# Optimization experiments

Measured on AMD Instinct MI355X. Metric: run time of the kernel, lower is better.

Reference implementation:

```python
import jax, jax.numpy as jnp
import numpy as np

NUM_HEADS = 16
HEAD_DIM = 64
EMB = 1024


def setup_inputs() -> dict:
    key = jax.random.key(0)
    k1, k2, k3 = jax.random.split(key, 3)
    x = jax.random.normal(k1, (4, 1024, EMB), dtype=jnp.float32)
    W_qkv = jax.random.normal(k2, (EMB, 3 * NUM_HEADS * HEAD_DIM), dtype=jnp.float32) * (EMB ** -0.5)
    b_qkv = jnp.zeros((3 * NUM_HEADS * HEAD_DIM,), dtype=jnp.float32)
    W_out = jax.random.normal(k3, (NUM_HEADS * HEAD_DIM, EMB), dtype=jnp.float32) * ((NUM_HEADS * HEAD_DIM) ** -0.5)
    b_out = jnp.zeros((EMB,), dtype=jnp.float32)
    return {"x": x, "W_qkv": W_qkv, "b_qkv": b_qkv, "W_out": W_out, "b_out": b_out}


def reference(x, W_qkv, b_qkv, W_out, b_out):
    B, N, D = x.shape
    qkv = x @ W_qkv + b_qkv                      # B N 3*H*hd
    # torch.split order in the source is K, Q, V
    K, Q, V = jnp.split(qkv, 3, axis=-1)
    def heads(t):  # B N (H hd) -> B H N hd
        return t.reshape(B, N, NUM_HEADS, HEAD_DIM).transpose(0, 2, 1, 3)
    K, Q, V = heads(K), heads(Q), heads(V)
    scores = jnp.einsum('bhqd,bhkd->bhqk', Q, K) / (HEAD_DIM ** 0.5)
    att = jax.nn.softmax(scores, axis=-1)        # dropout p=0.0 -> identity
    out = jnp.einsum('bhqk,bhkd->bhqd', att, V)  # B H N hd
    out = out.transpose(0, 2, 1, 3).reshape(B, N, NUM_HEADS * HEAD_DIM)
    return out @ W_out + b_out
```

## Files before the change

kernel.cpp:

```cpp
#include <hip/hip_runtime.h>
#include <hip/hip_bf16.h>
#include <cstddef>
#include <cmath>


typedef _Float16 f16x4 __attribute__((ext_vector_type(4)));
typedef _Float16 f16x8 __attribute__((ext_vector_type(8)));
typedef float    f32x4 __attribute__((ext_vector_type(4)));

#define LOG2E 1.4426950408889634f

__device__ __forceinline__ void gload_lds16(const void* g, void* l) {
    __builtin_amdgcn_global_load_lds(
        (const __attribute__((address_space(1))) unsigned int*)g,
        (__attribute__((address_space(3))) unsigned int*)l, 16, 0, 0);
}

__global__ __launch_bounds__(256) void cvt_f32_f16(
    const float* __restrict__ in, _Float16* __restrict__ out, int n8)
{
    int i = blockIdx.x * 256 + threadIdx.x;
    if (i < n8) {
        const float4* p = (const float4*)in;
        float4 v0 = p[i * 2], v1 = p[i * 2 + 1];
        f16x8 o;
        o[0] = (_Float16)v0.x; o[1] = (_Float16)v0.y; o[2] = (_Float16)v0.z; o[3] = (_Float16)v0.w;
        o[4] = (_Float16)v1.x; o[5] = (_Float16)v1.y; o[6] = (_Float16)v1.z; o[7] = (_Float16)v1.w;
        *(f16x8*)(out + (size_t)i * 8) = o;
    }
}

__global__ __launch_bounds__(256) void transpose_f32_to_f16(
    const float* __restrict__ in, _Float16* __restrict__ out, int R, int C)
{
    __shared__ float tile[64][65];
    int r0 = blockIdx.y * 64, c0 = blockIdx.x * 64;
    int t = threadIdx.x;
#pragma unroll
    for (int p = 0; p < 4; ++p) {
        int lin = p * 256 + t;
        int row = lin >> 4;
        int c4 = (lin & 15) * 4;
        float4 v = *(const float4*)(in + (size_t)(r0 + row) * C + c0 + c4);
        tile[row][c4] = v.x; tile[row][c4 + 1] = v.y;
        tile[row][c4 + 2] = v.z; tile[row][c4 + 3] = v.w;
    }
    __syncthreads();
#pragma unroll
    for (int p = 0; p < 2; ++p) {
        int lin = p * 256 + t;
        int oc = lin >> 3;
        int ch = (lin & 7) * 8;
        f16x8 o;
#pragma unroll
        for (int e = 0; e < 8; ++e) o[e] = (_Float16)tile[ch + e][oc];
        *(f16x8*)(out + (size_t)(c0 + oc) * R + r0 + ch) = o;
    }
}

__global__ __launch_bounds__(256) void transpose_f16(
    const _Float16* __restrict__ in, _Float16* __restrict__ out, int R, int C)
{
    __shared__ _Float16 tile[64][72];
    const _Float16* inh = in + (size_t)blockIdx.z * R * C;
    _Float16* outh = out + (size_t)blockIdx.z * R * C;
    int r0 = blockIdx.y * 64, c0 = blockIdx.x * 64;
    int t = threadIdx.x;
#pragma unroll
    for (int p = 0; p < 2; ++p) {
        int lin = p * 256 + t;
        int row = lin >> 3;
        int ch = (lin & 7) * 8;
        f16x8 v = *(const f16x8*)(inh + (size_t)(r0 + row) * C + c0 + ch);
        *(f16x8*)&tile[row][ch] = v;
    }
    __syncthreads();
#pragma unroll
    for (int p = 0; p < 2; ++p) {
        int lin = p * 256 + t;
        int oc = lin >> 3;
        int ch = (lin & 7) * 8;
        f16x8 o;
#pragma unroll
        for (int e = 0; e < 8; ++e) o[e] = tile[ch + e][oc];
        *(f16x8*)(outh + (size_t)(c0 + oc) * R + r0 + ch) = o;
    }
}

template <int EPI>
__global__ __launch_bounds__(512, 2) void gemm256(
    const _Float16* __restrict__ A, const _Float16* __restrict__ Bt,
    const float* __restrict__ bias, float* __restrict__ Cout,
    _Float16* __restrict__ Kh, _Float16* __restrict__ Qh, _Float16* __restrict__ Vh,
    int M, int Nn, int Kk)
{
    __shared__ _Float16 As[3][256 * 32];
    __shared__ _Float16 Bs[3][256 * 32];

    int lin = blockIdx.y * gridDim.x + blockIdx.x;
    int nwg = gridDim.x * gridDim.y;
    int lin2 = (lin & 7) * (nwg >> 3) + (lin >> 3);
    int bx = lin2 % gridDim.x, by = lin2 / gridDim.x;
    int m0 = by * 256, n0 = bx * 256;

    int tid = threadIdx.x, lane = tid & 63, wid = tid >> 6;
    int wm = wid >> 2, wn = wid & 3;
    int lr = lane & 15, lg = lane >> 4;

    int srow = tid >> 2;
    int scol = ((tid & 3) * 8) ^ ((srow & 6) << 2);
    const _Float16* pa0 = A  + (size_t)(m0 + srow) * Kk + scol;
    const _Float16* pa1 = A  + (size_t)(m0 + 128 + srow) * Kk + scol;
    const _Float16* pb0 = Bt + (size_t)(n0 + srow) * Kk + scol;
    const _Float16* pb1 = Bt + (size_t)(n0 + 128 + srow) * Kk + scol;
    int d0 = (wid * 64) * 8;
    int d1 = (512 + wid * 64) * 8;

    f32x4 acc[8][4] = {};
    const int NIT = Kk >> 5;

    {
        gload_lds16(pa0, &As[0][d0]); gload_lds16(pa1, &As[0][d1]);
        gload_lds16(pb0, &Bs[0][d0]); gload_lds16(pb1, &Bs[0][d1]);
        gload_lds16(pa0 + 32, &As[1][d0]); gload_lds16(pa1 + 32, &As[1][d1]);
        gload_lds16(pb0 + 32, &Bs[1][d0]); gload_lds16(pb1 + 32, &Bs[1][d1]);
    }

    for (int i = 0; i < NIT; ++i) {
        const _Float16* Ab = &As[i % 3][0];
        const _Float16* Bb = &Bs[i % 3][0];
        int sb = (i + 2) % 3;
        int ks = (i + 2 < NIT) ? (i + 2) * 32 : 0;

        asm volatile("s_waitcnt vmcnt(4)" ::: "memory");
        __builtin_amdgcn_s_barrier();

        f16x8 bf[4], af[4];
#pragma unroll
        for (int nf = 0; nf < 4; ++nf) {
            int rn = wn * 64 + nf * 16 + lr;
            bf[nf] = *(const f16x8*)&Bb[rn * 32 + ((lg * 8) ^ ((rn & 6) << 2))];
        }
#pragma unroll
        for (int mf = 0; mf < 4; ++mf) {
            int ra = wm * 128 + mf * 16 + lr;
            af[mf] = *(const f16x8*)&Ab[ra * 32 + ((lg * 8) ^ ((ra & 6) << 2))];
        }
        gload_lds16(pa0 + ks, &As[sb][d0]);
        gload_lds16(pa1 + ks, &As[sb][d1]);
        asm volatile("s_waitcnt lgkmcnt(0)" ::: "memory");
        __builtin_amdgcn_sched_barrier(0);
        __builtin_amdgcn_s_setprio(1);
#pragma unroll
        for (int mf = 0; mf < 4; ++mf)
#pragma unroll
            for (int nf = 0; nf < 4; ++nf)
                acc[mf][nf] = __builtin_amdgcn_mfma_f32_16x16x32_f16(
                    af[mf], bf[nf], acc[mf][nf], 0, 0, 0);
        __builtin_amdgcn_s_setprio(0);

#pragma unroll
        for (int mf = 0; mf < 4; ++mf) {
            int ra = wm * 128 + 64 + mf * 16 + lr;
            af[mf] = *(const f16x8*)&Ab[ra * 32 + ((lg * 8) ^ ((ra & 6) << 2))];
        }
        gload_lds16(pb0 + ks, &Bs[sb][d0]);
        gload_lds16(pb1 + ks, &Bs[sb][d1]);
        asm volatile("s_waitcnt lgkmcnt(0)" ::: "memory");
        __builtin_amdgcn_sched_barrier(0);
        __builtin_amdgcn_s_setprio(1);
#pragma unroll
        for (int mf = 0; mf < 4; ++mf)
#pragma unroll
            for (int nf = 0; nf < 4; ++nf)
                acc[4 + mf][nf] = __builtin_amdgcn_mfma_f32_16x16x32_f16(
                    af[mf], bf[nf], acc[4 + mf][nf], 0, 0, 0);
        __builtin_amdgcn_s_setprio(0);
    }

#pragma unroll
    for (int mh = 0; mh < 2; ++mh)
#pragma unroll
        for (int mf = 0; mf < 4; ++mf)
#pragma unroll
            for (int nf = 0; nf < 4; ++nf) {
                int gc = n0 + wn * 64 + nf * 16 + lr;
                float bv = bias[gc];
#pragma unroll
                for (int j = 0; j < 4; ++j) {
                    int gr = m0 + wm * 128 + mh * 64 + mf * 16 + lg * 4 + j;
                    float v = acc[mh * 4 + mf][nf][j] + bv;
                    if constexpr (EPI == 0) {
                        Cout[(size_t)gr * Nn + gc] = v;
                    } else {
                        int sec = gc >> 10, idx = gc & 1023;
                        int h = idx >> 6, d = idx & 63;
                        int bb = gr >> 10, pos = gr & 1023;
                        size_t hoff = (((size_t)(bb * 16 + h) * 1024) + pos) * 64 + d;
                        if (sec == 0)      Kh[hoff] = (_Float16)v;
                        else if (sec == 1) Qh[hoff] = (_Float16)(v * (0.125f * LOG2E));
                        else               Vh[hoff] = (_Float16)v;
                    }
                }
            }
}

template <int EPI>
__global__ __launch_bounds__(256) void gemm_f16(
    const _Float16* __restrict__ A, const _Float16* __restrict__ Bt,
    const float* __restrict__ bias, float* __restrict__ Cout,
    _Float16* __restrict__ Kh, _Float16* __restrict__ Qh, _Float16* __restrict__ Vh,
    int M, int Nn, int Kk)
{
    __shared__ _Float16 As[2][128 * 64];
    __shared__ _Float16 Bs[2][128 * 64];

    int lin = blockIdx.y * gridDim.x + blockIdx.x;
    int nwg = gridDim.x * gridDim.y;
    int lin2 = (lin & 7) * (nwg >> 3) + (lin >> 3);
    int bx = lin2 % gridDim.x, by = lin2 / gridDim.x;
    int m0 = by * 128, n0 = bx * 128;

    int t = threadIdx.x, lane = t & 63, wid = t >> 6;
    int wr = (wid >> 1) * 64, wc = (wid & 1) * 64;
    int lr = lane & 15, lg = lane >> 4;

    f32x4 acc[4][4] = {};
    int nt = Kk >> 6;

#pragma unroll
    for (int p = 0; p < 4; ++p) {
        int c = p * 256 + t;
        int row = c >> 3, col = (c & 7) * 8;
        int ubase = (p * 256 + wid * 64) * 8;
        gload_lds16(A  + (size_t)(m0 + row) * Kk + col, &As[0][ubase]);
        gload_lds16(Bt + (size_t)(n0 + row) * Kk + col, &Bs[0][ubase]);
    }
    __syncthreads();

    for (int tt = 0; tt < nt; ++tt) {
        int cur = tt & 1;
        if (tt + 1 < nt) {
            int k0 = (tt + 1) * 64;
#pragma unroll
            for (int p = 0; p < 4; ++p) {
                int c = p * 256 + t;
                int row = c >> 3, col = (c & 7) * 8;
                int ubase = (p * 256 + wid * 64) * 8;
                gload_lds16(A  + (size_t)(m0 + row) * Kk + k0 + col, &As[cur ^ 1][ubase]);
                gload_lds16(Bt + (size_t)(n0 + row) * Kk + k0 + col, &Bs[cur ^ 1][ubase]);
            }
        }
        const _Float16* Ac = &As[cur][0];
        const _Float16* Bc = &Bs[cur][0];
#pragma unroll
        for (int kk = 0; kk < 2; ++kk) {
            f16x8 af[4], bfr[4];
#pragma unroll
            for (int i = 0; i < 4; ++i) {
                af[i]  = *(const f16x8*)&Ac[(wr + i * 16 + lr) * 64 + kk * 32 + lg * 8];
                bfr[i] = *(const f16x8*)&Bc[(wc + i * 16 + lr) * 64 + kk * 32 + lg * 8];
            }
#pragma unroll
            for (int i = 0; i < 4; ++i)
#pragma unroll
                for (int jn = 0; jn < 4; ++jn)
                    acc[i][jn] = __builtin_amdgcn_mfma_f32_16x16x32_f16(
                        af[i], bfr[jn], acc[i][jn], 0, 0, 0);
        }
        __syncthreads();
    }

#pragma unroll
    for (int i = 0; i < 4; ++i)
#pragma unroll
        for (int jn = 0; jn < 4; ++jn) {
            int gc = n0 + wc + jn * 16 + lr;
            float bv = bias[gc];
#pragma unroll
            for (int j = 0; j < 4; ++j) {
                int gr = m0 + wr + i * 16 + lg * 4 + j;
                float v = acc[i][jn][j] + bv;
                if constexpr (EPI == 0) {
                    Cout[(size_t)gr * Nn + gc] = v;
                } else {
                    int sec = gc >> 10, idx = gc & 1023;
                    int h = idx >> 6, d = idx & 63;
                    int bb = gr >> 10, pos = gr & 1023;
                    size_t hoff = (((size_t)(bb * 16 + h) * 1024) + pos) * 64 + d;
                    if (sec == 0)      Kh[hoff] = (_Float16)v;
                    else if (sec == 1) Qh[hoff] = (_Float16)(v * (0.125f * LOG2E));
                    else               Vh[hoff] = (_Float16)v;
                }
            }
        }
}

__global__ __launch_bounds__(256) void attn_kernel(
    const _Float16* __restrict__ Qh, const _Float16* __restrict__ Kh,
    const _Float16* __restrict__ Vt, _Float16* __restrict__ attO)
{
    __shared__ _Float16 Ks[2][64 * 64];
    __shared__ _Float16 Vs[2][64 * 64];
    __shared__ _Float16 Pl[4][16 * 64];

    int wg = blockIdx.x;
    int swz = (wg & 7) * 128 + (wg >> 3);
    int bh = swz >> 4, qt = swz & 15;
    int b = bh >> 4, h = bh & 15;

    int tid = threadIdx.x;
    int wid = tid >> 6, lane = tid & 63;
    int lr = lane & 15, lg = lane >> 4;
    int q0 = qt * 64 + wid * 16;
    const _Float16* Qb = Qh + (size_t)bh * (1024 * 64);
    const _Float16* Kb = Kh + (size_t)bh * (1024 * 64);
    const _Float16* Vb = Vt + (size_t)bh * (64 * 1024);

    int c0 = tid, c1 = 256 + tid;
    int r0 = c0 >> 3, sc0 = ((c0 & 7) * 16) ^ ((r0 & 7) << 4);
    int r1 = c1 >> 3, sc1 = ((c1 & 7) * 16) ^ ((r1 & 7) << 4);
    int ub0 = (wid * 64) * 8, ub1 = (256 + wid * 64) * 8;

    f16x8 qf0 = *(const f16x8*)(Qb + (size_t)(q0 + lr) * 64 + lg * 8);
    f16x8 qf1 = *(const f16x8*)(Qb + (size_t)(q0 + lr) * 64 + 32 + lg * 8);

    float m = -1e30f, l = 0.f;
    f32x4 o[4] = {};
    int xr = (lr & 7) << 4;

    gload_lds16(Kb + (size_t)r0 * 64 + (sc0 >> 1), &Ks[0][ub0]);
    gload_lds16(Kb + (size_t)r1 * 64 + (sc1 >> 1), &Ks[0][ub1]);
    gload_lds16(Vb + (size_t)r0 * 1024 + (sc0 >> 1), &Vs[0][ub0]);
    gload_lds16(Vb + (size_t)r1 * 1024 + (sc1 >> 1), &Vs[0][ub1]);
    __syncthreads();

    for (int t = 0; t < 16; ++t) {
        int cur = t & 1;
        if (t < 15) {
            int kn = (t + 1) * 64;
            gload_lds16(Kb + (size_t)(kn + r0) * 64 + (sc0 >> 1), &Ks[cur ^ 1][ub0]);
            gload_lds16(Kb + (size_t)(kn + r1) * 64 + (sc1 >> 1), &Ks[cur ^ 1][ub1]);
            gload_lds16(Vb + (size_t)r0 * 1024 + kn + (sc0 >> 1), &Vs[cur ^ 1][ub0]);
            gload_lds16(Vb + (size_t)r1 * 1024 + kn + (sc1 >> 1), &Vs[cur ^ 1][ub1]);
        }
        const _Float16* Kc = &Ks[cur][0];
        const _Float16* Vc = &Vs[cur][0];

        f32x4 s[4] = {};
#pragma unroll
        for (int kb = 0; kb < 4; ++kb) {
            const char* krow = (const char*)(Kc + (kb * 16 + lr) * 64);
            f16x8 kf0 = *(const f16x8*)(krow + ((lg * 16) ^ xr));
            f16x8 kf1 = *(const f16x8*)(krow + ((64 + lg * 16) ^ xr));
            s[kb] = __builtin_amdgcn_mfma_f32_16x16x32_f16(kf0, qf0, s[kb], 0, 0, 0);
            s[kb] = __builtin_amdgcn_mfma_f32_16x16x32_f16(kf1, qf1, s[kb], 0, 0, 0);
        }
        float a0 = fmaxf(fmaxf(s[0][0], s[0][1]), fmaxf(s[0][2], s[0][3]));
        float a1 = fmaxf(fmaxf(s[1][0], s[1][1]), fmaxf(s[1][2], s[1][3]));
        float a2 = fmaxf(fmaxf(s[2][0], s[2][1]), fmaxf(s[2][2], s[2][3]));
        float a3 = fmaxf(fmaxf(s[3][0], s[3][1]), fmaxf(s[3][2], s[3][3]));
        float pmax = fmaxf(fmaxf(a0, a1), fmaxf(a2, a3));
        pmax = fmaxf(pmax, __shfl_xor(pmax, 16));
        pmax = fmaxf(pmax, __shfl_xor(pmax, 32));
        float mnew = fmaxf(m, pmax);
        float corr = exp2f(m - mnew);
#pragma unroll
        for (int kb = 0; kb < 4; ++kb)
#pragma unroll
            for (int j = 0; j < 4; ++j)
                s[kb][j] = exp2f(s[kb][j] - mnew);
        float rr0 = (s[0][0] + s[0][1]) + (s[0][2] + s[0][3]);
        float rr1 = (s[1][0] + s[1][1]) + (s[1][2] + s[1][3]);
        float rr2 = (s[2][0] + s[2][1]) + (s[2][2] + s[2][3]);
        float rr3 = (s[3][0] + s[3][1]) + (s[3][2] + s[3][3]);
        float rs = (rr0 + rr1) + (rr2 + rr3);
        rs += __shfl_xor(rs, 16);
        rs += __shfl_xor(rs, 32);
        l = l * corr + rs;
        m = mnew;
#pragma unroll
        for (int db = 0; db < 4; ++db)
#pragma unroll
            for (int j = 0; j < 4; ++j) o[db][j] *= corr;

        char* prow = (char*)&Pl[wid][lr * 64];
#pragma unroll
        for (int kb = 0; kb < 4; ++kb) {
            f16x4 w;
#pragma unroll
            for (int j = 0; j < 4; ++j) w[j] = (_Float16)s[kb][j];
            *(f16x4*)(prow + ((kb * 32 + lg * 8) ^ xr)) = w;
        }
        f16x8 pf0 = *(const f16x8*)(prow + ((lg * 16) ^ xr));
        f16x8 pf1 = *(const f16x8*)(prow + ((64 + lg * 16) ^ xr));

#pragma unroll
        for (int db = 0; db < 4; ++db) {
            const char* vrow = (const char*)(Vc + (db * 16 + lr) * 64);
            f16x8 vf0 = *(const f16x8*)(vrow + ((lg * 16) ^ xr));
            f16x8 vf1 = *(const f16x8*)(vrow + ((64 + lg * 16) ^ xr));
            o[db] = __builtin_amdgcn_mfma_f32_16x16x32_f16(vf0, pf0, o[db], 0, 0, 0);
            o[db] = __builtin_amdgcn_mfma_f32_16x16x32_f16(vf1, pf1, o[db], 0, 0, 0);
        }
        __syncthreads();
    }

    float li = 1.f / l;
#pragma unroll
    for (int db = 0; db < 4; ++db) {
        f16x4 w;
#pragma unroll
        for (int j = 0; j < 4; ++j) w[j] = (_Float16)(o[db][j] * li);
        *(f16x4*)(attO + ((size_t)b * 1024 + q0 + lr) * 1024 + h * 64 + db * 16 + lg * 4) = w;
    }
}

extern "C" void kernel_launch(void* const* d_in, const int* in_sizes, int n_in,
                              void* d_out, int out_size, void* d_ws, size_t ws_size,
                              hipStream_t stream)
{
    const float* x    = (const float*)d_in[0];
    const float* Wqkv = (const float*)d_in[1];
    const float* bqkv = (const float*)d_in[2];
    const float* Wout = (const float*)d_in[3];
    const float* bout = (const float*)d_in[4];
    float* out = (float*)d_out;

    char* ws = (char*)d_ws;
    _Float16* xb    = (_Float16*)(ws);
    _Float16* Vt    = (_Float16*)(ws);
    _Float16* Wqkvt = (_Float16*)(ws + ((size_t)8  << 20));
    _Float16* Woutt = (_Float16*)(ws + ((size_t)14 << 20));
    _Float16* Qh    = (_Float16*)(ws + ((size_t)16 << 20));
    _Float16* Kh    = (_Float16*)(ws + ((size_t)24 << 20));
    _Float16* Vh    = (_Float16*)(ws + ((size_t)32 << 20));
    _Float16* attO  = (_Float16*)(ws + ((size_t)40 << 20));

    cvt_f32_f16<<<2048, 256, 0, stream>>>(x, xb, 4096 * 1024 / 8);
    transpose_f32_to_f16<<<dim3(48, 16), 256, 0, stream>>>(Wqkv, Wqkvt, 1024, 3072);
    transpose_f32_to_f16<<<dim3(16, 16), 256, 0, stream>>>(Wout, Woutt, 1024, 1024);

    gemm256<1><<<dim3(12, 16), 512, 0, stream>>>(
        xb, Wqkvt, bqkv, nullptr, Kh, Qh, Vh, 4096, 3072, 1024);

    transpose_f16<<<dim3(1, 16, 64), 256, 0, stream>>>(Vh, Vt, 1024, 64);

    attn_kernel<<<1024, 256, 0, stream>>>(Qh, Kh, Vt, attO);

    gemm_f16<0><<<dim3(8, 32), 256, 0, stream>>>(
        attO, Woutt, bout, out, nullptr, nullptr, nullptr, 4096, 1024, 1024);
}
```

Before: 190.9 us.

## Fuse prep kernels, write V transposed from QKV GEMM, tune attention loop

Merges the x conversion and both weight transposes into one prep launch. The QKV GEMM epilogue now writes V directly in transposed layout with packed f16x4 stores, which removes the separate V transpose kernel and its round trip through memory. The attention kernel hoists its LDS offsets, skips the rescale when the row max is unchanged for the whole wave, uses packed RTZ conversion for P, raises wave priority around the MFMA blocks and unrolls the loop by two. This cuts launches and memory traffic, but RTZ rounding changes numerics slightly, and the wave-uniform skip adds a branch.

```diff
diff --git a/kernel.cpp b/kernel.cpp
--- a/kernel.cpp
+++ b/kernel.cpp
@@ -6,6 +6,7 @@
 
 typedef _Float16 f16x4 __attribute__((ext_vector_type(4)));
 typedef _Float16 f16x8 __attribute__((ext_vector_type(8)));
+typedef __fp16   fp16x2r __attribute__((ext_vector_type(2)));
 typedef float    f32x4 __attribute__((ext_vector_type(4)));
 
 #define LOG2E 1.4426950408889634f
@@ -16,26 +17,11 @@
         (__attribute__((address_space(3))) unsigned int*)l, 16, 0, 0);
 }
 
-__global__ __launch_bounds__(256) void cvt_f32_f16(
-    const float* __restrict__ in, _Float16* __restrict__ out, int n8)
-{
-    int i = blockIdx.x * 256 + threadIdx.x;
-    if (i < n8) {
-        const float4* p = (const float4*)in;
-        float4 v0 = p[i * 2], v1 = p[i * 2 + 1];
-        f16x8 o;
-        o[0] = (_Float16)v0.x; o[1] = (_Float16)v0.y; o[2] = (_Float16)v0.z; o[3] = (_Float16)v0.w;
-        o[4] = (_Float16)v1.x; o[5] = (_Float16)v1.y; o[6] = (_Float16)v1.z; o[7] = (_Float16)v1.w;
-        *(f16x8*)(out + (size_t)i * 8) = o;
-    }
-}
-
-__global__ __launch_bounds__(256) void transpose_f32_to_f16(
-    const float* __restrict__ in, _Float16* __restrict__ out, int R, int C)
-{
-    __shared__ float tile[64][65];
-    int r0 = blockIdx.y * 64, c0 = blockIdx.x * 64;
-    int t = threadIdx.x;
+__device__ __forceinline__ void transpose_tile_f32f16(
+    const float* __restrict__ in, _Float16* __restrict__ out,
+    int R, int C, int cx, int cy, int t, float (*tile)[65])
+{
+    int r0 = cy * 64, c0 = cx * 64;
 #pragma unroll
     for (int p = 0; p < 4; ++p) {
         int lin = p * 256 + t;
@@ -58,32 +44,27 @@
     }
 }
 
-__global__ __launch_bounds__(256) void transpose_f16(
-    const _Float16* __restrict__ in, _Float16* __restrict__ out, int R, int C)
-{
-    __shared__ _Float16 tile[64][72];
-    const _Float16* inh = in + (size_t)blockIdx.z * R * C;
-    _Float16* outh = out + (size_t)blockIdx.z * R * C;
-    int r0 = blockIdx.y * 64, c0 = blockIdx.x * 64;
-    int t = threadIdx.x;
-#pragma unroll
-    for (int p = 0; p < 2; ++p) {
-        int lin = p * 256 + t;
-        int row = lin >> 3;
-        int ch = (lin & 7) * 8;
-        f16x8 v = *(const f16x8*)(inh + (size_t)(r0 + row) * C + c0 + ch);
-        *(f16x8*)&tile[row][ch] = v;
-    }
-    __syncthreads();
-#pragma unroll
-    for (int p = 0; p < 2; ++p) {
-        int lin = p * 256 + t;
-        int oc = lin >> 3;
-        int ch = (lin & 7) * 8;
+__global__ __launch_bounds__(256) void prep(
+    const float* __restrict__ x, _Float16* __restrict__ xb,
+    const float* __restrict__ Wqkv, _Float16* __restrict__ Wqkvt,
+    const float* __restrict__ Wout, _Float16* __restrict__ Woutt)
+{
+    __shared__ float tile[64][65];
+    int bid = blockIdx.x, t = threadIdx.x;
+    if (bid < 2048) {
+        int i = bid * 256 + t;
+        const float4* p = (const float4*)x;
+        float4 v0 = p[i * 2], v1 = p[i * 2 + 1];
         f16x8 o;
-#pragma unroll
-        for (int e = 0; e < 8; ++e) o[e] = tile[ch + e][oc];
-        *(f16x8*)(outh + (size_t)(c0 + oc) * R + r0 + ch) = o;
+        o[0] = (_Float16)v0.x; o[1] = (_Float16)v0.y; o[2] = (_Float16)v0.z; o[3] = (_Float16)v0.w;
+        o[4] = (_Float16)v1.x; o[5] = (_Float16)v1.y; o[6] = (_Float16)v1.z; o[7] = (_Float16)v1.w;
+        *(f16x8*)(xb + (size_t)i * 8) = o;
+    } else if (bid < 2816) {
+        int id = bid - 2048;
+        transpose_tile_f32f16(Wqkv, Wqkvt, 1024, 3072, id % 48, id / 48, t, tile);
+    } else {
+        int id = bid - 2816;
+        transpose_tile_f32f16(Wout, Woutt, 1024, 1024, id % 16, id / 16, t, tile);
     }
 }
 
@@ -91,7 +72,7 @@
 __global__ __launch_bounds__(512, 2) void gemm256(
     const _Float16* __restrict__ A, const _Float16* __restrict__ Bt,
     const float* __restrict__ bias, float* __restrict__ Cout,
-    _Float16* __restrict__ Kh, _Float16* __restrict__ Qh, _Float16* __restrict__ Vh,
+    _Float16* __restrict__ Kh, _Float16* __restrict__ Qh, _Float16* __restrict__ Vtd,
     int M, int Nn, int Kk)
 {
     __shared__ _Float16 As[3][256 * 32];
@@ -119,12 +100,10 @@
     f32x4 acc[8][4] = {};
     const int NIT = Kk >> 5;
 
-    {
-        gload_lds16(pa0, &As[0][d0]); gload_lds16(pa1, &As[0][d1]);
-        gload_lds16(pb0, &Bs[0][d0]); gload_lds16(pb1, &Bs[0][d1]);
-        gload_lds16(pa0 + 32, &As[1][d0]); gload_lds16(pa1 + 32, &As[1][d1]);
-        gload_lds16(pb0 + 32, &Bs[1][d0]); gload_lds16(pb1 + 32, &Bs[1][d1]);
-    }
+    gload_lds16(pa0, &As[0][d0]); gload_lds16(pa1, &As[0][d1]);
+    gload_lds16(pb0, &Bs[0][d0]); gload_lds16(pb1, &Bs[0][d1]);
+    gload_lds16(pa0 + 32, &As[1][d0]); gload_lds16(pa1 + 32, &As[1][d1]);
+    gload_lds16(pb0 + 32, &Bs[1][d0]); gload_lds16(pb1 + 32, &Bs[1][d1]);
 
     for (int i = 0; i < NIT; ++i) {
         const _Float16* Ab = &As[i % 3][0];
@@ -181,35 +160,47 @@
 #pragma unroll
     for (int mh = 0; mh < 2; ++mh)
 #pragma unroll
-        for (int mf = 0; mf < 4; ++mf)
+        for (int mf = 0; mf < 4; ++mf) {
+            int gr0 = m0 + wm * 128 + mh * 64 + mf * 16 + lg * 4;
+            int bb = gr0 >> 10, pos = gr0 & 1023;
 #pragma unroll
             for (int nf = 0; nf < 4; ++nf) {
                 int gc = n0 + wn * 64 + nf * 16 + lr;
                 float bv = bias[gc];
-#pragma unroll
-                for (int j = 0; j < 4; ++j) {
-                    int gr = m0 + wm * 128 + mh * 64 + mf * 16 + lg * 4 + j;
-                    float v = acc[mh * 4 + mf][nf][j] + bv;
-                    if constexpr (EPI == 0) {
-                        Cout[(size_t)gr * Nn + gc] = v;
+                const f32x4& a = acc[mh * 4 + mf][nf];
+                if constexpr (EPI == 0) {
+#pragma unroll
+                    for (int j = 0; j < 4; ++j)
+                        Cout[(size_t)(gr0 + j) * Nn + gc] = a[j] + bv;
+                } else {
+                    int sec = gc >> 10, idx = gc & 1023;
+                    int h = idx >> 6, d = idx & 63;
+                    if (sec == 2) {
+                        f16x4 w;
+#pragma unroll
+                        for (int j = 0; j < 4; ++j) w[j] = (_Float16)(a[j] + bv);
+                        *(f16x4*)&Vtd[(((size_t)(bb * 16 + h)) * 64 + d) * 1024 + pos] = w;
                     } else {
-                        int sec = gc >> 10, idx = gc & 1023;
-                        int h = idx >> 6, d = idx & 63;
-                        int bb = gr >> 10, pos = gr & 1023;
-                        size_t hoff = (((size_t)(bb * 16 + h) * 1024) + pos) * 64 + d;
-                        if (sec == 0)      Kh[hoff] = (_Float16)v;
-                        else if (sec == 1) Qh[hoff] = (_Float16)(v * (0.125f * LOG2E));
-                        else               Vh[hoff] = (_Float16)v;
+                        size_t base = (((size_t)(bb * 16 + h)) * 1024 + pos) * 64 + d;
+                        if (sec == 0) {
+#pragma unroll
+                            for (int j = 0; j < 4; ++j)
+                                Kh[base + (size_t)j * 64] = (_Float16)(a[j] + bv);
+                        } else {
+#pragma unroll
+                            for (int j = 0; j < 4; ++j)
+                                Qh[base + (size_t)j * 64] = (_Float16)((a[j] + bv) * (0.125f * LOG2E));
+                        }
                     }
                 }
             }
+        }
 }
 
 template <int EPI>
 __global__ __launch_bounds__(256) void gemm_f16(
     const _Float16* __restrict__ A, const _Float16* __restrict__ Bt,
     const float* __restrict__ bias, float* __restrict__ Cout,
-    _Float16* __restrict__ Kh, _Float16* __restrict__ Qh, _Float16* __restrict__ Vh,
     int M, int Nn, int Kk)
 {
     __shared__ _Float16 As[2][128 * 64];
@@ -280,18 +271,7 @@
 #pragma unroll
             for (int j = 0; j < 4; ++j) {
                 int gr = m0 + wr + i * 16 + lg * 4 + j;
-                float v = acc[i][jn][j] + bv;
-                if constexpr (EPI == 0) {
-                    Cout[(size_t)gr * Nn + gc] = v;
-                } else {
-                    int sec = gc >> 10, idx = gc & 1023;
-                    int h = idx >> 6, d = idx & 63;
-                    int bb = gr >> 10, pos = gr & 1023;
-                    size_t hoff = (((size_t)(bb * 16 + h) * 1024) + pos) * 64 + d;
-                    if (sec == 0)      Kh[hoff] = (_Float16)v;
-                    else if (sec == 1) Qh[hoff] = (_Float16)(v * (0.125f * LOG2E));
-                    else               Vh[hoff] = (_Float16)v;
-                }
+                Cout[(size_t)gr * Nn + gc] = acc[i][jn][j] + bv;
             }
         }
 }
@@ -328,6 +308,9 @@
     float m = -1e30f, l = 0.f;
     f32x4 o[4] = {};
     int xr = (lr & 7) << 4;
+    int ko0 = lr * 128 + ((lg * 16) ^ xr);
+    int ko1 = lr * 128 + ((64 + lg * 16) ^ xr);
+    char* prow = (char*)&Pl[wid][lr * 64];
 
     gload_lds16(Kb + (size_t)r0 * 64 + (sc0 >> 1), &Ks[0][ub0]);
     gload_lds16(Kb + (size_t)r1 * 64 + (sc1 >> 1), &Ks[0][ub1]);
@@ -335,6 +318,7 @@
     gload_lds16(Vb + (size_t)r1 * 1024 + (sc1 >> 1), &Vs[0][ub1]);
     __syncthreads();
 
+#pragma unroll 2
     for (int t = 0; t < 16; ++t) {
         int cur = t & 1;
         if (t < 15) {
@@ -344,18 +328,20 @@
             gload_lds16(Vb + (size_t)r0 * 1024 + kn + (sc0 >> 1), &Vs[cur ^ 1][ub0]);
             gload_lds16(Vb + (size_t)r1 * 1024 + kn + (sc1 >> 1), &Vs[cur ^ 1][ub1]);
         }
-        const _Float16* Kc = &Ks[cur][0];
-        const _Float16* Vc = &Vs[cur][0];
+        const char* Kc = (const char*)&Ks[cur][0];
+        const char* Vc = (const char*)&Vs[cur][0];
 
         f32x4 s[4] = {};
+        __builtin_amdgcn_s_setprio(1);
 #pragma unroll
         for (int kb = 0; kb < 4; ++kb) {
-            const char* krow = (const char*)(Kc + (kb * 16 + lr) * 64);
-            f16x8 kf0 = *(const f16x8*)(krow + ((lg * 16) ^ xr));
-            f16x8 kf1 = *(const f16x8*)(krow + ((64 + lg * 16) ^ xr));
+            f16x8 kf0 = *(const f16x8*)(Kc + kb * 2048 + ko0);
+            f16x8 kf1 = *(const f16x8*)(Kc + kb * 2048 + ko1);
             s[kb] = __builtin_amdgcn_mfma_f32_16x16x32_f16(kf0, qf0, s[kb], 0, 0, 0);
             s[kb] = __builtin_amdgcn_mfma_f32_16x16x32_f16(kf1, qf1, s[kb], 0, 0, 0);
         }
+        __builtin_amdgcn_s_setprio(0);
+
         float a0 = fmaxf(fmaxf(s[0][0], s[0][1]), fmaxf(s[0][2], s[0][3]));
         float a1 = fmaxf(fmaxf(s[1][0], s[1][1]), fmaxf(s[1][2], s[1][3]));
         float a2 = fmaxf(fmaxf(s[2][0], s[2][1]), fmaxf(s[2][2], s[2][3]));
@@ -363,13 +349,22 @@
         float pmax = fmaxf(fmaxf(a0, a1), fmaxf(a2, a3));
         pmax = fmaxf(pmax, __shfl_xor(pmax, 16));
         pmax = fmaxf(pmax, __shfl_xor(pmax, 32));
-        float mnew = fmaxf(m, pmax);
-        float corr = exp2f(m - mnew);
+
+        if (!__all(pmax <= m)) {
+            float mnew = fmaxf(m, pmax);
+            float corr = exp2f(m - mnew);
+            l *= corr;
+#pragma unroll
+            for (int db = 0; db < 4; ++db)
+#pragma unroll
+                for (int j = 0; j < 4; ++j) o[db][j] *= corr;
+            m = mnew;
+        }
 #pragma unroll
         for (int kb = 0; kb < 4; ++kb)
 #pragma unroll
             for (int j = 0; j < 4; ++j)
-                s[kb][j] = exp2f(s[kb][j] - mnew);
+                s[kb][j] = exp2f(s[kb][j] - m);
         float rr0 = (s[0][0] + s[0][1]) + (s[0][2] + s[0][3]);
         float rr1 = (s[1][0] + s[1][1]) + (s[1][2] + s[1][3]);
         float rr2 = (s[2][0] + s[2][1]) + (s[2][2] + s[2][3]);
@@ -377,32 +372,27 @@
         float rs = (rr0 + rr1) + (rr2 + rr3);
         rs += __shfl_xor(rs, 16);
         rs += __shfl_xor(rs, 32);
-        l = l * corr + rs;
-        m = mnew;
-#pragma unroll
-        for (int db = 0; db < 4; ++db)
-#pragma unroll
-            for (int j = 0; j < 4; ++j) o[db][j] *= corr;
-
-        char* prow = (char*)&Pl[wid][lr * 64];
+        l += rs;
+
 #pragma unroll
         for (int kb = 0; kb < 4; ++kb) {
-            f16x4 w;
-#pragma unroll
-            for (int j = 0; j < 4; ++j) w[j] = (_Float16)s[kb][j];
-            *(f16x4*)(prow + ((kb * 32 + lg * 8) ^ xr)) = w;
+            union { fp16x2r hp[2]; uint2 u; } cv;
+            cv.hp[0] = __builtin_amdgcn_cvt_pkrtz(s[kb][0], s[kb][1]);
+            cv.hp[1] = __builtin_amdgcn_cvt_pkrtz(s[kb][2], s[kb][3]);
+            *(uint2*)(prow + ((kb * 32 + lg * 8) ^ xr)) = cv.u;
         }
         f16x8 pf0 = *(const f16x8*)(prow + ((lg * 16) ^ xr));
         f16x8 pf1 = *(const f16x8*)(prow + ((64 + lg * 16) ^ xr));
 
+        __builtin_amdgcn_s_setprio(1);
 #pragma unroll
         for (int db = 0; db < 4; ++db) {
-            const char* vrow = (const char*)(Vc + (db * 16 + lr) * 64);
-            f16x8 vf0 = *(const f16x8*)(vrow + ((lg * 16) ^ xr));
-            f16x8 vf1 = *(const f16x8*)(vrow + ((64 + lg * 16) ^ xr));
+            f16x8 vf0 = *(const f16x8*)(Vc + db * 2048 + ko0);
+            f16x8 vf1 = *(const f16x8*)(Vc + db * 2048 + ko1);
             o[db] = __builtin_amdgcn_mfma_f32_16x16x32_f16(vf0, pf0, o[db], 0, 0, 0);
             o[db] = __builtin_amdgcn_mfma_f32_16x16x32_f16(vf1, pf1, o[db], 0, 0, 0);
         }
+        __builtin_amdgcn_s_setprio(0);
         __syncthreads();
     }
 
@@ -429,25 +419,20 @@
 
     char* ws = (char*)d_ws;
     _Float16* xb    = (_Float16*)(ws);
-    _Float16* Vt    = (_Float16*)(ws);
     _Float16* Wqkvt = (_Float16*)(ws + ((size_t)8  << 20));
     _Float16* Woutt = (_Float16*)(ws + ((size_t)14 << 20));
     _Float16* Qh    = (_Float16*)(ws + ((size_t)16 << 20));
     _Float16* Kh    = (_Float16*)(ws + ((size_t)24 << 20));
-    _Float16* Vh    = (_Float16*)(ws + ((size_t)32 << 20));
+    _Float16* Vt    = (_Float16*)(ws + ((size_t)32 << 20));
     _Float16* attO  = (_Float16*)(ws + ((size_t)40 << 20));
 
-    cvt_f32_f16<<<2048, 256, 0, stream>>>(x, xb, 4096 * 1024 / 8);
-    transpose_f32_to_f16<<<dim3(48, 16), 256, 0, stream>>>(Wqkv, Wqkvt, 1024, 3072);
-    transpose_f32_to_f16<<<dim3(16, 16), 256, 0, stream>>>(Wout, Woutt, 1024, 1024);
+    prep<<<3072, 256, 0, stream>>>(x, xb, Wqkv, Wqkvt, Wout, Woutt);
 
     gemm256<1><<<dim3(12, 16), 512, 0, stream>>>(
-        xb, Wqkvt, bqkv, nullptr, Kh, Qh, Vh, 4096, 3072, 1024);
-
-    transpose_f16<<<dim3(1, 16, 64), 256, 0, stream>>>(Vh, Vt, 1024, 64);
+        xb, Wqkvt, bqkv, nullptr, Kh, Qh, Vt, 4096, 3072, 1024);
 
     attn_kernel<<<1024, 256, 0, stream>>>(Qh, Kh, Vt, attO);
 
     gemm_f16<0><<<dim3(8, 32), 256, 0, stream>>>(
-        attO, Woutt, bout, out, nullptr, nullptr, nullptr, 4096, 1024, 1024);
-}
+        attO, Woutt, bout, out, 4096, 1024, 1024);
+}
```

Measured after the change: 184.5 us. 1.04x faster.
